# Kernel optimization log

Measured on AMD Instinct MI355X. Metric: run time of the kernel, lower is better.

## Reference

```python
import jax, jax.numpy as jnp
import numpy as np

H = 51  # hidden size hard-coded in the module

def _lstm_cell(x_t, h, c, W_ih, W_hh, b_ih, b_hh):
    # PyTorch LSTMCell gate order: i, f, g, o
    gates = x_t @ W_ih.T + b_ih + h @ W_hh.T + b_hh  # [B, 4H]
    i, f, g, o = jnp.split(gates, 4, axis=-1)
    c_new = jax.nn.sigmoid(f) * c + jax.nn.sigmoid(i) * jnp.tanh(g)
    h_new = jax.nn.sigmoid(o) * jnp.tanh(c_new)
    return h_new, c_new


def setup_inputs() -> dict:
    key = jax.random.key(0)
    ks = jax.random.split(key, 11)
    B, T = 4096, 1024
    s = 1.0 / np.sqrt(H)
    return {
        "x": jax.random.normal(ks[0], (B, T), jnp.float32),
        "W_ih1": jax.random.uniform(ks[1], (4 * H, 1), jnp.float32, -s, s),
        "W_hh1": jax.random.uniform(ks[2], (4 * H, H), jnp.float32, -s, s),
        "b_ih1": jax.random.uniform(ks[3], (4 * H,), jnp.float32, -s, s),
        "b_hh1": jax.random.uniform(ks[4], (4 * H,), jnp.float32, -s, s),
        "W_ih2": jax.random.uniform(ks[5], (4 * H, H), jnp.float32, -s, s),
        "W_hh2": jax.random.uniform(ks[6], (4 * H, H), jnp.float32, -s, s),
        "b_ih2": jax.random.uniform(ks[7], (4 * H,), jnp.float32, -s, s),
        "b_hh2": jax.random.uniform(ks[8], (4 * H,), jnp.float32, -s, s),
        "W_lin": jax.random.uniform(ks[9], (1, H), jnp.float32, -s, s),
        "b_lin": jax.random.uniform(ks[10], (1,), jnp.float32, -s, s),
        "future": 64,
    }


def reference(x, W_ih1, W_hh1, b_ih1, b_hh1, W_ih2, W_hh2, b_ih2, b_hh2, W_lin, b_lin, future):
    B = x.shape[0]
    zeros = jnp.zeros((B, H), x.dtype)

    def step(carry, x_t):
        h1, c1, h2, c2 = carry
        h1, c1 = _lstm_cell(x_t, h1, c1, W_ih1, W_hh1, b_ih1, b_hh1)
        h2, c2 = _lstm_cell(h1, h2, c2, W_ih2, W_hh2, b_ih2, b_hh2)
        out = h2 @ W_lin.T + b_lin  # [B, 1]
        return (h1, c1, h2, c2), out

    xs = x.T[:, :, None]  # [T, B, 1]
    carry, outs = jax.lax.scan(step, (zeros, zeros, zeros, zeros), xs)

    def fut_step(carry, _):
        (h1, c1, h2, c2), out = carry
        h1, c1 = _lstm_cell(out, h1, c1, W_ih1, W_hh1, b_ih1, b_hh1)
        h2, c2 = _lstm_cell(h1, h2, c2, W_ih2, W_hh2, b_ih2, b_hh2)
        out = h2 @ W_lin.T + b_lin
        return ((h1, c1, h2, c2), out), out

    if future > 0:
        last_out = outs[-1]
        _, fut_outs = jax.lax.scan(fut_step, (carry, last_out), None, length=future)
        outs = jnp.concatenate([outs, fut_outs], axis=0)  # [T+future, B, 1]

    return outs[:, :, 0].T  # [B, T+future]
```

## Files before the change

### kernel.cpp

```cpp
#include <hip/hip_runtime.h>

#define HH    51
#define T_SEQ 1024
#define T_TOT 1088
#define B_TOT 4096
#define MT    16
#define NTH   512

typedef __attribute__((ext_vector_type(8))) short bf8_t;
typedef __attribute__((ext_vector_type(4))) float f32x4;

#define H1H_O 0
#define H1L_O 4096
#define H2H_O 8192
#define H2L_O 12288
#define XB_O  16384
#define OB_O  18432
#define PT_O  20480
#define SM_SZ 20992

#define L2E 1.44269504088896f

#if __has_builtin(__builtin_amdgcn_exp2f)
#define FEXP2 __builtin_amdgcn_exp2f
#else
#define FEXP2 exp2f
#endif
#if __has_builtin(__builtin_amdgcn_rcpf)
#define FRCP __builtin_amdgcn_rcpf
#else
#define FRCP(v) (1.f / (v))
#endif

__device__ __forceinline__ short f2bf(float f) {
  unsigned u = __builtin_bit_cast(unsigned, f);
  u += 0x7fffu + ((u >> 16) & 1u);
  return (short)(u >> 16);
}
__device__ __forceinline__ float bf2f(short s) {
  unsigned u = ((unsigned)(unsigned short)s) << 16;
  return __builtin_bit_cast(float, u);
}
__device__ __forceinline__ float lsig(float v) { return FRCP(1.f + FEXP2(v)); }

__device__ __forceinline__ f32x4 MFMA(bf8_t a, bf8_t b, f32x4 c) {
  return __builtin_amdgcn_mfma_f32_16x16x32_bf16(a, b, c, 0, 0, 0);
}
__device__ __forceinline__ bf8_t ldA(const char* base, int row, int off) {
  off ^= ((row & 7) << 4);
  return *reinterpret_cast<const bf8_t*>(base + row * 128 + off);
}
__device__ __forceinline__ void sthl(char* WH, char* WL, int row, int boff, float v) {
  const int o = row * 128 + (boff ^ ((row & 7) << 4));
  const unsigned u = __builtin_bit_cast(unsigned, v);
  *reinterpret_cast<short*>(WH + o) = (short)(u >> 16);
  const float rem = v - __builtin_bit_cast(float, u & 0xffff0000u);
  *reinterpret_cast<short*>(WL + o) = (short)(__builtin_bit_cast(unsigned, rem) >> 16);
}

__global__ __launch_bounds__(NTH, 1)
void lstm_mfma_kernel(const float* __restrict__ x,
                      const float* __restrict__ Wih1, const float* __restrict__ Whh1,
                      const float* __restrict__ bih1, const float* __restrict__ bhh1,
                      const float* __restrict__ Wih2, const float* __restrict__ Whh2,
                      const float* __restrict__ bih2, const float* __restrict__ bhh2,
                      const float* __restrict__ Wlin, const float* __restrict__ blin,
                      float* __restrict__ out)
{
  extern __shared__ char smc[];
  float* smf = (float*)smc;
  const int tid  = threadIdx.x;
  const int lane = tid & 63;
  const int w    = tid >> 6;
  const int cl   = lane & 15;
  const int gr   = lane >> 4;
  const int rng  = w & 3;
  const bool isL2 = (w >= 4);
  const int jo   = rng * 16 + cl;
  const bool jv  = (jo < HH);
  const int bg0  = blockIdx.x * MT;

  for (int i = tid; i < SM_SZ / 4; i += NTH) smf[i] = 0.f;

  const float gsc[4] = {-L2E, -L2E, 2.f * L2E, -L2E};

  bf8_t Bh[4][4], Bl[4][4];
  #pragma unroll
  for (int g = 0; g < 4; ++g) {
    #pragma unroll
    for (int kb = 0; kb < 4; ++kb) {
      bf8_t vh, vl;
      const bool dead = (!isL2 && kb >= 2);
      const float* Wsrc = isL2 ? (kb < 2 ? Wih2 : Whh2) : Whh1;
      const int kbase = (kb & 1) * 32;
      #pragma unroll
      for (int s = 0; s < 8; ++s) {
        const int ku = kbase + gr * 8 + s;
        float v = (!dead && jv && ku < HH) ? Wsrc[(g * HH + jo) * HH + ku] * gsc[g] : 0.f;
        const short hh = f2bf(v);
        vh[s] = hh;
        vl[s] = f2bf(v - bf2f(hh));
      }
      Bh[g][kb] = vh; Bl[g][kb] = vl;
    }
  }
  float cbv[4], wih1v[4];
  #pragma unroll
  for (int g = 0; g < 4; ++g) {
    cbv[g]   = jv ? (isL2 ? (bih2[g*HH+jo] + bhh2[g*HH+jo])
                          : (bih1[g*HH+jo] + bhh1[g*HH+jo])) * gsc[g] : 0.f;
    wih1v[g] = (jv && !isL2) ? Wih1[g*HH+jo] * gsc[g] : 0.f;
  }
  const float wlv = (jv && isL2) ? Wlin[jo] : 0.f;
  const float bl  = blin[0];
  float cst[4] = {0.f, 0.f, 0.f, 0.f};

  auto act_h = [&](const f32x4 acc[4], int r) -> float {
    const float si = lsig(acc[0][r]);
    const float sf = lsig(acc[1][r]);
    const float tg = 1.f - 2.f * lsig(acc[2][r]);
    const float so = lsig(acc[3][r]);
    const float cn = sf * cst[r] + si * tg;
    cst[r] = cn;
    return so * (1.f - 2.f * lsig(cn * (2.f * L2E)));
  };

  auto do_l1 = [&](const int p, const float xv[4]) {
    const char* RH = smc + H1H_O + (p ^ 1) * 2048;
    const char* RL = smc + H1L_O + (p ^ 1) * 2048;
    bf8_t a0 = ldA(RH, cl, gr*16), a1 = ldA(RH, cl, 64 + gr*16);
    bf8_t l0 = ldA(RL, cl, gr*16), l1 = ldA(RL, cl, 64 + gr*16);
    f32x4 acc[4];
    #pragma unroll
    for (int g = 0; g < 4; ++g) {
      f32x4 a = {cbv[g], cbv[g], cbv[g], cbv[g]};
      a = MFMA(a0, Bh[g][0], a); a = MFMA(a1, Bh[g][1], a);
      a = MFMA(l0, Bh[g][0], a); a = MFMA(l1, Bh[g][1], a);
      a = MFMA(a0, Bl[g][0], a); a = MFMA(a1, Bl[g][1], a);
      acc[g] = a;
    }
    #pragma unroll
    for (int g = 0; g < 4; ++g)
      #pragma unroll
      for (int r = 0; r < 4; ++r) acc[g][r] += wih1v[g] * xv[r];
    char* WH = smc + H1H_O + p * 2048;
    char* WL = smc + H1L_O + p * 2048;
    #pragma unroll
    for (int r = 0; r < 4; ++r) {
      const float hv = act_h(acc, r);
      if (jv) sthl(WH, WL, gr * 4 + r, 2 * jo, hv);
    }
  };

  auto do_l2 = [&](const int q) {
    const char* R1H = smc + H1H_O + q * 2048,       *R1L = smc + H1L_O + q * 2048;
    const char* R2H = smc + H2H_O + (q ^ 1) * 2048, *R2L = smc + H2L_O + (q ^ 1) * 2048;
    bf8_t a[4], al[4];
    a[0]  = ldA(R1H, cl, gr*16); a[1]  = ldA(R1H, cl, 64 + gr*16);
    a[2]  = ldA(R2H, cl, gr*16); a[3]  = ldA(R2H, cl, 64 + gr*16);
    al[0] = ldA(R1L, cl, gr*16); al[1] = ldA(R1L, cl, 64 + gr*16);
    al[2] = ldA(R2L, cl, gr*16); al[3] = ldA(R2L, cl, 64 + gr*16);
    f32x4 acc[4];
    #pragma unroll
    for (int g = 0; g < 4; ++g) {
      f32x4 ac = {cbv[g], cbv[g], cbv[g], cbv[g]};
      #pragma unroll
      for (int kb = 0; kb < 4; ++kb) ac = MFMA(a[kb],  Bh[g][kb], ac);
      #pragma unroll
      for (int kb = 0; kb < 4; ++kb) ac = MFMA(al[kb], Bh[g][kb], ac);
      #pragma unroll
      for (int kb = 0; kb < 4; ++kb) ac = MFMA(a[kb],  Bl[g][kb], ac);
      acc[g] = ac;
    }
    char* WH = smc + H2H_O + q * 2048;
    char* WL = smc + H2L_O + q * 2048;
    float po[4];
    #pragma unroll
    for (int r = 0; r < 4; ++r) {
      const float hv = act_h(acc, r);
      if (jv) sthl(WH, WL, gr * 4 + r, 2 * jo, hv);
      po[r] = wlv * hv;
    }
    #pragma unroll
    for (int r = 0; r < 4; ++r) {
      #pragma unroll
      for (int m = 1; m < 16; m <<= 1) po[r] += __shfl_xor(po[r], m, 64);
    }
    if (cl == 0) {
      #pragma unroll
      for (int r = 0; r < 4; ++r)
        smf[PT_O/4 + q*64 + rng*16 + gr*4 + r] = po[r];
    }
  };

  auto finalize = [&](int tw, const int q, float ov[4]) {
    #pragma unroll
    for (int r = 0; r < 4; ++r) {
      const int row = gr * 4 + r;
      ov[r] = smf[PT_O/4 + q*64 +  0 + row] + smf[PT_O/4 + q*64 + 16 + row]
            + smf[PT_O/4 + q*64 + 32 + row] + smf[PT_O/4 + q*64 + 48 + row] + bl;
    }
    (void)tw;
  };
  auto writeOB = [&](int tw, const float ov[4]) {
    if (cl == 0) {
      const int po = (tw >> 4) & 1, cc = tw & 15;
      #pragma unroll
      for (int r = 0; r < 4; ++r)
        smf[OB_O/4 + po*256 + (gr*4 + r)*16 + cc] = ov[r];
    }
  };
  auto flushOB = [&](int tb) {
    const int q = (tb >> 4) & 1;
    #pragma unroll
    for (int it = 0; it < 4; ++it) {
      const int idx = lane + 64 * it;
      const int r = idx >> 4, tt = idx & 15;
      out[(size_t)(bg0 + r) * T_TOT + tb + tt] = smf[OB_O/4 + q*256 + r*16 + tt];
    }
  };

  __syncthreads();
  if (tid < 256) {
    const int r = tid >> 4, tt = tid & 15;
    smf[XB_O/4 + r*16 + tt] = x[(size_t)(bg0 + r) * T_SEQ + tt];
  }
  __syncthreads();

  auto main_step = [&](int t, const int p) {
    if (!isL2) {
      if (w == 0 && t >= 2) { float ov[4]; finalize(t - 2, p, ov); writeOB(t - 2, ov); }
      if ((w == 1 || w == 2) && (t & 15) == 0 && (t + 16) < T_SEQ) {
        const int nt = t + 16, par = (nt >> 4) & 1;
        #pragma unroll
        for (int it = 0; it < 2; ++it) {
          const int idx = (w - 1) * 128 + lane + 64 * it;
          const int r = idx >> 4, tt = idx & 15;
          smf[XB_O/4 + par*256 + r*16 + tt] = x[(size_t)(bg0 + r) * T_SEQ + nt + tt];
        }
      }
      if (w == 3 && (t & 15) == 9 && t >= 25) flushOB(((t - 2) & ~15) - 16);
      float xv[4];
      const int par = (t >> 4) & 1, cc = t & 15;
      #pragma unroll
      for (int r = 0; r < 4; ++r) xv[r] = smf[XB_O/4 + par*256 + (gr*4 + r)*16 + cc];
      do_l1(p, xv);
    } else {
      if (t >= 1) do_l2(p ^ 1);
    }
  };

  #pragma unroll 1
  for (int t = 0; t < T_SEQ; t += 2) {
    main_step(t, 0);
    __syncthreads();
    main_step(t + 1, 1);
    __syncthreads();
  }
  if (isL2) do_l2(1);
  else if (w == 0) { float ov[4]; finalize(T_SEQ - 2, 0, ov); writeOB(T_SEQ - 2, ov); }
  __syncthreads();

  auto ar_step = [&](int t, const int p) {
    if (!isL2) {
      float ov[4];
      finalize(t - 1, p ^ 1, ov);
      if (w == 0) writeOB(t - 1, ov);
      if (w == 3 && (t & 15) == 8) flushOB(((t - 1) & ~15) - 16);
      do_l1(p, ov);
    }
    __syncthreads();
    if (isL2) do_l2(p);
    __syncthreads();
  };
  #pragma unroll 1
  for (int t = T_SEQ; t < T_TOT; t += 2) {
    ar_step(t, 0);
    ar_step(t + 1, 1);
  }
  if (!isL2 && w == 0) { float ov[4]; finalize(T_TOT - 1, 1, ov); writeOB(T_TOT - 1, ov); }
  __syncthreads();
  if (w == 3) flushOB(T_TOT - 16);
}

extern "C" void kernel_launch(void* const* d_in, const int* in_sizes, int n_in,
                              void* d_out, int out_size, void* d_ws, size_t ws_size,
                              hipStream_t stream) {
  const float* x    = (const float*)d_in[0];
  const float* Wih1 = (const float*)d_in[1];
  const float* Whh1 = (const float*)d_in[2];
  const float* bih1 = (const float*)d_in[3];
  const float* bhh1 = (const float*)d_in[4];
  const float* Wih2 = (const float*)d_in[5];
  const float* Whh2 = (const float*)d_in[6];
  const float* bih2 = (const float*)d_in[7];
  const float* bhh2 = (const float*)d_in[8];
  const float* Wlin = (const float*)d_in[9];
  const float* blin = (const float*)d_in[10];
  float* out = (float*)d_out;

  lstm_mfma_kernel<<<B_TOT / MT, NTH, SM_SZ, stream>>>(
      x, Wih1, Whh1, bih1, bhh1, Wih2, Whh2, bih2, bhh2, Wlin, blin, out);
}
```

Before: 1.492 ms.

## Fold input and output projections into MFMAs and raise MFMA wave priority

```diff
diff --git a/kernel.cpp b/kernel.cpp
--- a/kernel.cpp
+++ b/kernel.cpp
@@ -97,12 +97,26 @@
       for (int s = 0; s < 8; ++s) {
         const int ku = kbase + gr * 8 + s;
         float v = (!dead && jv && ku < HH) ? Wsrc[(g * HH + jo) * HH + ku] * gsc[g] : 0.f;
+        if (!isL2 && kb == 1 && ku == 53) v = jv ? Wih1[g * HH + jo] * gsc[g] : 0.f;
         const short hh = f2bf(v);
         vh[s] = hh;
         vl[s] = f2bf(v - bf2f(hh));
       }
       Bh[g][kb] = vh; Bl[g][kb] = vl;
     }
+  }
+  bf8_t Bo[2];
+  #pragma unroll
+  for (int kb = 0; kb < 2; ++kb) {
+    bf8_t v;
+    #pragma unroll
+    for (int s = 0; s < 8; ++s) {
+      const int ku = kb * 32 + gr * 8 + s;
+      float wv = (ku < HH) ? Wlin[ku] : 0.f;
+      const short hh = f2bf(wv);
+      v[s] = (cl == 0) ? hh : (cl == 1) ? f2bf(wv - bf2f(hh)) : (short)0;
+    }
+    Bo[kb] = v;
   }
   float cbv[4], wih1v[4];
   #pragma unroll
@@ -125,12 +139,22 @@
     return so * (1.f - 2.f * lsig(cn * (2.f * L2E)));
   };
 
-  auto do_l1 = [&](const int p, const float xv[4]) {
+  auto writeOB = [&](int tw, const float ov[4]) {
+    if (cl == 0) {
+      const int po = (tw >> 4) & 1, cc = tw & 15;
+      #pragma unroll
+      for (int r = 0; r < 4; ++r)
+        smf[OB_O/4 + po*256 + (gr*4 + r)*16 + cc] = ov[r];
+    }
+  };
+
+  auto do_l1 = [&](const int p, const float* xv, const int t) {
     const char* RH = smc + H1H_O + (p ^ 1) * 2048;
     const char* RL = smc + H1L_O + (p ^ 1) * 2048;
     bf8_t a0 = ldA(RH, cl, gr*16), a1 = ldA(RH, cl, 64 + gr*16);
     bf8_t l0 = ldA(RL, cl, gr*16), l1 = ldA(RL, cl, 64 + gr*16);
     f32x4 acc[4];
+    __builtin_amdgcn_s_setprio(1);
     #pragma unroll
     for (int g = 0; g < 4; ++g) {
       f32x4 a = {cbv[g], cbv[g], cbv[g], cbv[g]};
@@ -139,10 +163,13 @@
       a = MFMA(a0, Bl[g][0], a); a = MFMA(a1, Bl[g][1], a);
       acc[g] = a;
     }
-    #pragma unroll
-    for (int g = 0; g < 4; ++g)
-      #pragma unroll
-      for (int r = 0; r < 4; ++r) acc[g][r] += wih1v[g] * xv[r];
+    __builtin_amdgcn_s_setprio(0);
+    if (xv) {
+      #pragma unroll
+      for (int g = 0; g < 4; ++g)
+        #pragma unroll
+        for (int r = 0; r < 4; ++r) acc[g][r] += wih1v[g] * xv[r];
+    }
     char* WH = smc + H1H_O + p * 2048;
     char* WL = smc + H1L_O + p * 2048;
     #pragma unroll
@@ -150,9 +177,15 @@
       const float hv = act_h(acc, r);
       if (jv) sthl(WH, WL, gr * 4 + r, 2 * jo, hv);
     }
-  };
-
-  auto do_l2 = [&](const int q) {
+    if (!xv && rng == 3 && (t + 1) < T_SEQ) {
+      if (lane < 16) {
+        const float xn = smf[XB_O/4 + (((t+1) >> 4) & 1) * 256 + lane * 16 + ((t+1) & 15)];
+        sthl(WH, WL, lane, 2 * 53, xn);
+      }
+    }
+  };
+
+  auto do_l2 = [&](const int q, const bool ar, const int tw) {
     const char* R1H = smc + H1H_O + q * 2048,       *R1L = smc + H1L_O + q * 2048;
     const char* R2H = smc + H2H_O + (q ^ 1) * 2048, *R2L = smc + H2L_O + (q ^ 1) * 2048;
     bf8_t a[4], al[4];
@@ -161,6 +194,8 @@
     al[0] = ldA(R1L, cl, gr*16); al[1] = ldA(R1L, cl, 64 + gr*16);
     al[2] = ldA(R2L, cl, gr*16); al[3] = ldA(R2L, cl, 64 + gr*16);
     f32x4 acc[4];
+    f32x4 d = {0.f, 0.f, 0.f, 0.f};
+    __builtin_amdgcn_s_setprio(1);
     #pragma unroll
     for (int g = 0; g < 4; ++g) {
       f32x4 ac = {cbv[g], cbv[g], cbv[g], cbv[g]};
@@ -172,6 +207,11 @@
       for (int kb = 0; kb < 4; ++kb) ac = MFMA(a[kb],  Bl[g][kb], ac);
       acc[g] = ac;
     }
+    if (!ar && rng == 0) {
+      d = MFMA(a[3], Bo[1], d); d = MFMA(a[2], Bo[0], d);
+      d = MFMA(al[3], Bo[1], d); d = MFMA(al[2], Bo[0], d);
+    }
+    __builtin_amdgcn_s_setprio(0);
     char* WH = smc + H2H_O + q * 2048;
     char* WL = smc + H2L_O + q * 2048;
     float po[4];
@@ -181,34 +221,34 @@
       if (jv) sthl(WH, WL, gr * 4 + r, 2 * jo, hv);
       po[r] = wlv * hv;
     }
-    #pragma unroll
-    for (int r = 0; r < 4; ++r) {
-      #pragma unroll
-      for (int m = 1; m < 16; m <<= 1) po[r] += __shfl_xor(po[r], m, 64);
-    }
-    if (cl == 0) {
-      #pragma unroll
-      for (int r = 0; r < 4; ++r)
-        smf[PT_O/4 + q*64 + rng*16 + gr*4 + r] = po[r];
-    }
-  };
-
-  auto finalize = [&](int tw, const int q, float ov[4]) {
+    if (!ar) {
+      if (rng == 0 && tw >= 0) {
+        float ov[4];
+        #pragma unroll
+        for (int r = 0; r < 4; ++r) ov[r] = d[r] + __shfl_xor(d[r], 1, 64) + bl;
+        writeOB(tw, ov);
+      }
+    } else {
+      #pragma unroll
+      for (int r = 0; r < 4; ++r) {
+        #pragma unroll
+        for (int m = 1; m < 16; m <<= 1) po[r] += __shfl_xor(po[r], m, 64);
+      }
+      if (cl == 0) {
+        #pragma unroll
+        for (int r = 0; r < 4; ++r)
+          smf[PT_O/4 + q*64 + rng*16 + gr*4 + r] = po[r];
+      }
+    }
+  };
+
+  auto finalize = [&](const int q, float ov[4]) {
     #pragma unroll
     for (int r = 0; r < 4; ++r) {
       const int row = gr * 4 + r;
       ov[r] = smf[PT_O/4 + q*64 +  0 + row] + smf[PT_O/4 + q*64 + 16 + row]
             + smf[PT_O/4 + q*64 + 32 + row] + smf[PT_O/4 + q*64 + 48 + row] + bl;
     }
-    (void)tw;
-  };
-  auto writeOB = [&](int tw, const float ov[4]) {
-    if (cl == 0) {
-      const int po = (tw >> 4) & 1, cc = tw & 15;
-      #pragma unroll
-      for (int r = 0; r < 4; ++r)
-        smf[OB_O/4 + po*256 + (gr*4 + r)*16 + cc] = ov[r];
-    }
   };
   auto flushOB = [&](int tb) {
     const int q = (tb >> 4) & 1;
@@ -225,11 +265,13 @@
     const int r = tid >> 4, tt = tid & 15;
     smf[XB_O/4 + r*16 + tt] = x[(size_t)(bg0 + r) * T_SEQ + tt];
   }
+  if (tid < 16)
+    sthl(smc + H1H_O + 2048, smc + H1L_O + 2048, tid, 2 * 53,
+         x[(size_t)(bg0 + tid) * T_SEQ]);
   __syncthreads();
 
   auto main_step = [&](int t, const int p) {
     if (!isL2) {
-      if (w == 0 && t >= 2) { float ov[4]; finalize(t - 2, p, ov); writeOB(t - 2, ov); }
       if ((w == 1 || w == 2) && (t & 15) == 0 && (t + 16) < T_SEQ) {
         const int nt = t + 16, par = (nt >> 4) & 1;
         #pragma unroll
@@ -240,13 +282,9 @@
         }
       }
       if (w == 3 && (t & 15) == 9 && t >= 25) flushOB(((t - 2) & ~15) - 16);
-      float xv[4];
-      const int par = (t >> 4) & 1, cc = t & 15;
-      #pragma unroll
-      for (int r = 0; r < 4; ++r) xv[r] = smf[XB_O/4 + par*256 + (gr*4 + r)*16 + cc];
-      do_l1(p, xv);
+      do_l1(p, nullptr, t);
     } else {
-      if (t >= 1) do_l2(p ^ 1);
+      if (t >= 1) do_l2(p ^ 1, false, t - 2);
     }
   };
 
@@ -257,20 +295,37 @@
     main_step(t + 1, 1);
     __syncthreads();
   }
-  if (isL2) do_l2(1);
-  else if (w == 0) { float ov[4]; finalize(T_SEQ - 2, 0, ov); writeOB(T_SEQ - 2, ov); }
+  if (isL2) {
+    do_l2(1, true, -1);
+    if (rng == 0) {
+      const char* RH = smc + H2H_O;
+      const char* RL = smc + H2L_O;
+      bf8_t a2 = ldA(RH, cl, gr*16), a3 = ldA(RH, cl, 64 + gr*16);
+      bf8_t b2 = ldA(RL, cl, gr*16), b3 = ldA(RL, cl, 64 + gr*16);
+      f32x4 d = {0.f, 0.f, 0.f, 0.f};
+      d = MFMA(a3, Bo[1], d); d = MFMA(a2, Bo[0], d);
+      d = MFMA(b3, Bo[1], d); d = MFMA(b2, Bo[0], d);
+      float ov[4];
+      #pragma unroll
+      for (int r = 0; r < 4; ++r) ov[r] = d[r] + __shfl_xor(d[r], 1, 64) + bl;
+      writeOB(1022, ov);
+    }
+  } else if (w == 3 && lane < 16) {
+    sthl(smc + H1H_O,        smc + H1L_O,        lane, 2 * 53, 0.f);
+    sthl(smc + H1H_O + 2048, smc + H1L_O + 2048, lane, 2 * 53, 0.f);
+  }
   __syncthreads();
 
   auto ar_step = [&](int t, const int p) {
     if (!isL2) {
       float ov[4];
-      finalize(t - 1, p ^ 1, ov);
+      finalize(p ^ 1, ov);
       if (w == 0) writeOB(t - 1, ov);
       if (w == 3 && (t & 15) == 8) flushOB(((t - 1) & ~15) - 16);
-      do_l1(p, ov);
+      do_l1(p, ov, t);
     }
     __syncthreads();
-    if (isL2) do_l2(p);
+    if (isL2) do_l2(p, true, -1);
     __syncthreads();
   };
   #pragma unroll 1
@@ -278,7 +333,7 @@
     ar_step(t, 0);
     ar_step(t + 1, 1);
   }
-  if (!isL2 && w == 0) { float ov[4]; finalize(T_TOT - 1, 1, ov); writeOB(T_TOT - 1, ov); }
+  if (!isL2 && w == 0) { float ov[4]; finalize(1, ov); writeOB(T_TOT - 1, ov); }
   __syncthreads();
   if (w == 3) flushOB(T_TOT - 16);
 }
```

Result: faster. 1.293 ms (-13.3%).
